# Optimization experiments

Measured on AMD Instinct MI355X. Metric: run time of the kernel, lower is better.

Reference implementation:

```python
import jax, jax.numpy as jnp
import numpy as np

N_POINTS = 200000
C_IN = 64
C_OUT = 64
K_VOL = 27  # 3x3x3 kernel offsets
N_PAIRS = 100000  # neighbor pairs per kernel offset
BN_EPS = 1e-5


def setup_inputs() -> dict:
    key = jax.random.key(0)
    k1, k2, k3, k4 = jax.random.split(key, 4)
    feats = jax.random.normal(k1, (N_POINTS, C_IN), dtype=jnp.float32)
    in_map = jax.random.randint(k2, (K_VOL, N_PAIRS), 0, N_POINTS, dtype=jnp.int32)
    out_map = jax.random.randint(k3, (K_VOL, N_PAIRS), 0, N_POINTS, dtype=jnp.int32)
    # learned params: conv kernel [K, Cin, Cout], BN affine + running stats
    kernel = jax.random.normal(k4, (K_VOL, C_IN, C_OUT), dtype=jnp.float32) * (1.0 / np.sqrt(C_IN * K_VOL))
    gamma = jnp.ones((C_OUT,), dtype=jnp.float32)
    beta = jnp.zeros((C_OUT,), dtype=jnp.float32)
    running_mean = jnp.zeros((C_OUT,), dtype=jnp.float32)
    running_var = jnp.ones((C_OUT,), dtype=jnp.float32)
    return {
        "feats": feats,
        "kernel": kernel,
        "gamma": gamma,
        "beta": beta,
        "running_mean": running_mean,
        "running_var": running_var,
        "in_map": in_map,
        "out_map": out_map,
    }


def reference(feats, kernel, gamma, beta, running_mean, running_var, in_map, out_map):
    # Sparse conv as gather -> per-offset GEMM -> scatter-add (torchsparse semantics)
    n = feats.shape[0]
    c_out = kernel.shape[-1]
    gathered = feats[in_map]                                   # [K, M, Cin]
    contrib = jnp.einsum('kmc,kco->kmo', gathered, kernel)     # [K, M, Cout]
    out = jnp.zeros((n, c_out), dtype=feats.dtype)
    out = out.at[out_map.reshape(-1)].add(contrib.reshape(-1, c_out))
    # BatchNorm (inference: fold running stats into scale/bias) + ReLU epilogue
    scale = gamma * jax.lax.rsqrt(running_var + BN_EPS)        # [Cout]
    out = out * scale + (beta - running_mean * scale)
    return jax.nn.relu(out)
```

## Files before the change

### kernel.cpp

```cpp
#include <hip/hip_runtime.h>
#include <hip/hip_bf16.h>

#define NPTS 200000
#define CIN 64
#define COUT 64
#define KVOL 27
#define NPAIRS 100000
#define GROUPS_PER_K (NPAIRS / 16)
#define GROUPS_PER_BLOCK 64
#define CHUNKS_PER_K ((GROUPS_PER_K + GROUPS_PER_BLOCK - 1) / GROUPS_PER_BLOCK)
#define BN_EPS 1e-5f

typedef __attribute__((ext_vector_type(8))) short short8;
typedef __attribute__((ext_vector_type(4))) float f32x4;

__device__ inline ushort f2bf(float x) {
    union { __hip_bfloat16 h; ushort u; } cv;
    cv.h = __float2bfloat16(x);
    return cv.u;
}

__global__ __launch_bounds__(256) void conv_scatter_kernel(
    const float* __restrict__ feats,
    const float* __restrict__ wk,
    const int* __restrict__ in_map,
    const int* __restrict__ out_map,
    float* __restrict__ accum)
{
    const int koff  = blockIdx.x / CHUNKS_PER_K;
    const int chunk = blockIdx.x % CHUNKS_PER_K;
    const int lane  = threadIdx.x & 63;
    const int wave  = threadIdx.x >> 6;
    const int m     = lane & 15;
    const int q     = lane >> 4;

    short8 bfrag[2][4];
    const float* wbase = wk + koff * (CIN * COUT);
    #pragma unroll
    for (int h = 0; h < 2; ++h) {
        #pragma unroll
        for (int nt = 0; nt < 4; ++nt) {
            #pragma unroll
            for (int e = 0; e < 8; ++e) {
                const int kin = h * 32 + q * 8 + e;
                bfrag[h][nt][e] = (short)f2bf(wbase[kin * COUT + nt * 16 + m]);
            }
        }
    }

    const int* imap = in_map + koff * NPAIRS;
    const int* omap = out_map + koff * NPAIRS;

    #pragma unroll 1
    for (int it = 0; it < GROUPS_PER_BLOCK / 4; ++it) {
        const int g = chunk * GROUPS_PER_BLOCK + it * 4 + wave;
        if (g >= GROUPS_PER_K) break;
        const int base = g * 16;

        const int row = imap[base + m];
        const float* fr = feats + (size_t)row * CIN + q * 8;
        const f32x4 f00 = *(const f32x4*)(fr);
        const f32x4 f01 = *(const f32x4*)(fr + 4);
        const f32x4 f10 = *(const f32x4*)(fr + 32);
        const f32x4 f11 = *(const f32x4*)(fr + 36);

        short8 a0, a1;
        #pragma unroll
        for (int e = 0; e < 4; ++e) {
            a0[e]     = (short)f2bf(f00[e]);
            a0[e + 4] = (short)f2bf(f01[e]);
            a1[e]     = (short)f2bf(f10[e]);
            a1[e + 4] = (short)f2bf(f11[e]);
        }

        f32x4 acc[4];
        #pragma unroll
        for (int nt = 0; nt < 4; ++nt) acc[nt] = (f32x4){0.f, 0.f, 0.f, 0.f};
        #pragma unroll
        for (int nt = 0; nt < 4; ++nt) {
            acc[nt] = __builtin_amdgcn_mfma_f32_16x16x32_bf16(a0, bfrag[0][nt], acc[nt], 0, 0, 0);
            acc[nt] = __builtin_amdgcn_mfma_f32_16x16x32_bf16(a1, bfrag[1][nt], acc[nt], 0, 0, 0);
        }

        int orow[4];
        #pragma unroll
        for (int r = 0; r < 4; ++r) orow[r] = omap[base + q * 4 + r];

        #pragma unroll
        for (int nt = 0; nt < 4; ++nt) {
            #pragma unroll
            for (int r = 0; r < 4; ++r) {
                unsafeAtomicAdd(accum + (size_t)orow[r] * COUT + nt * 16 + m, acc[nt][r]);
            }
        }
    }
}

__global__ __launch_bounds__(256) void bn_relu_kernel(
    const float* __restrict__ accum,
    const float* __restrict__ gamma,
    const float* __restrict__ beta,
    const float* __restrict__ rmean,
    const float* __restrict__ rvar,
    float* __restrict__ out)
{
    __shared__ float s_scale[COUT];
    __shared__ float s_bias[COUT];
    if (threadIdx.x < COUT) {
        const int c = threadIdx.x;
        const float sc = gamma[c] * rsqrtf(rvar[c] + BN_EPS);
        s_scale[c] = sc;
        s_bias[c]  = beta[c] - rmean[c] * sc;
    }
    __syncthreads();

    const int idx = (blockIdx.x * 256 + threadIdx.x) * 4;
    if (idx < NPTS * COUT) {
        const f32x4 v = *(const f32x4*)(accum + idx);
        const int c0 = idx & (COUT - 1);
        f32x4 o;
        #pragma unroll
        for (int e = 0; e < 4; ++e) {
            o[e] = fmaxf(v[e] * s_scale[c0 + e] + s_bias[c0 + e], 0.f);
        }
        *(f32x4*)(out + idx) = o;
    }
}

extern "C" void kernel_launch(void* const* d_in, const int* in_sizes, int n_in,
                              void* d_out, int out_size, void* d_ws, size_t ws_size,
                              hipStream_t stream) {
    const float* feats = (const float*)d_in[0];
    const float* wk    = (const float*)d_in[1];
    const float* gamma = (const float*)d_in[2];
    const float* beta  = (const float*)d_in[3];
    const float* rmean = (const float*)d_in[4];
    const float* rvar  = (const float*)d_in[5];
    const int* imap    = (const int*)d_in[6];
    const int* omap    = (const int*)d_in[7];
    float* out         = (float*)d_out;
    float* accum       = (float*)d_ws;

    hipMemsetAsync(accum, 0, (size_t)NPTS * COUT * sizeof(float), stream);

    conv_scatter_kernel<<<KVOL * CHUNKS_PER_K, 256, 0, stream>>>(feats, wk, imap, omap, accum);

    bn_relu_kernel<<<(NPTS * COUT / 4 + 255) / 256, 256, 0, stream>>>(
        accum, gamma, beta, rmean, rvar, out);
}
```

Baseline: 677.7 us.

## Replace global atomic scatter with output-tile bucketing and LDS gather-accumulate

Builds a counting-sort of neighbor pairs keyed by (16-row output tile, kernel offset) using a histogram, three-stage prefix scan and fill pass, then runs a gather-style conv where each wave owns one output tile and accumulates into LDS with shared-memory atomics. BN+ReLU is fused into the tile write-out, and weights are pre-transposed to bf16 once. This removes the 256MB-scale global float atomics, the memset and the separate BN pass. The cost is several extra small kernels, global integer atomics for bucketing, and partially filled MFMA groups, since buckets average about 8 pairs per 16-row slot.

Result: slower. 1.378 ms (+103.4%).

```diff
diff --git a/kernel.cpp b/kernel.cpp
--- a/kernel.cpp
+++ b/kernel.cpp
@@ -6,10 +6,16 @@
 #define COUT 64
 #define KVOL 27
 #define NPAIRS 100000
-#define GROUPS_PER_K (NPAIRS / 16)
-#define GROUPS_PER_BLOCK 64
-#define CHUNKS_PER_K ((GROUPS_PER_K + GROUPS_PER_BLOCK - 1) / GROUPS_PER_BLOCK)
+#define NPAIRS_TOT (KVOL * NPAIRS)
+#define NTILES (NPTS / 16)
+#define NKEYS (NTILES * KVOL)
+#define SCAN_ITEMS 2048
+#define NSCANB ((NKEYS + SCAN_ITEMS - 1) / SCAN_ITEMS)
 #define BN_EPS 1e-5f
+
+static_assert(NPTS % 16 == 0, "tiles");
+static_assert(NTILES % 4 == 0, "4 waves/block");
+static_assert(NSCANB <= 256, "single-block top scan");
 
 typedef __attribute__((ext_vector_type(8))) short short8;
 typedef __attribute__((ext_vector_type(4))) float f32x4;
@@ -20,110 +26,185 @@
     return cv.u;
 }
 
-__global__ __launch_bounds__(256) void conv_scatter_kernel(
+
+__global__ __launch_bounds__(256) void wprep_kernel(const float* __restrict__ wk,
+                                                    ushort* __restrict__ wt) {
+    const int i = blockIdx.x * 256 + threadIdx.x;
+    if (i >= KVOL * CIN * COUT) return;
+    const int k = i >> 12, r = i & 4095, co = r >> 6, ci = r & 63;
+    wt[i] = f2bf(wk[(k << 12) | (ci << 6) | co]);
+}
+
+__global__ __launch_bounds__(256) void hist_kernel(const int* __restrict__ omap,
+                                                   int* __restrict__ cnt) {
+    for (int i = blockIdx.x * 256 + threadIdx.x; i < NPAIRS_TOT; i += gridDim.x * 256) {
+        const int k = i / NPAIRS;
+        atomicAdd(&cnt[(omap[i] >> 4) * KVOL + k], 1);
+    }
+}
+
+__global__ __launch_bounds__(256) void scan1_kernel(const int* __restrict__ cnt,
+                                                    int* __restrict__ offs,
+                                                    int* __restrict__ bsum) {
+    __shared__ int s[256];
+    const int t = threadIdx.x;
+    const int base = blockIdx.x * SCAN_ITEMS + t * 8;
+    int v[8]; int sum = 0;
+    #pragma unroll
+    for (int i = 0; i < 8; ++i) {
+        const int idx = base + i;
+        v[i] = (idx < NKEYS) ? cnt[idx] : 0;
+        sum += v[i];
+    }
+    s[t] = sum;
+    __syncthreads();
+    for (int off = 1; off < 256; off <<= 1) {
+        const int x = (t >= off) ? s[t - off] : 0;
+        __syncthreads();
+        s[t] += x;
+        __syncthreads();
+    }
+    if (t == 255) bsum[blockIdx.x] = s[255];
+    int run = s[t] - sum;
+    #pragma unroll
+    for (int i = 0; i < 8; ++i) {
+        const int idx = base + i;
+        if (idx < NKEYS) offs[idx] = run;
+        run += v[i];
+    }
+}
+
+__global__ __launch_bounds__(256) void scan2_kernel(int* __restrict__ bsum) {
+    __shared__ int s[256];
+    const int t = threadIdx.x;
+    const int v = (t < NSCANB) ? bsum[t] : 0;
+    s[t] = v;
+    __syncthreads();
+    for (int off = 1; off < 256; off <<= 1) {
+        const int x = (t >= off) ? s[t - off] : 0;
+        __syncthreads();
+        s[t] += x;
+        __syncthreads();
+    }
+    if (t < NSCANB) bsum[t] = s[t] - v;
+}
+
+__global__ __launch_bounds__(256) void scan3_kernel(int* __restrict__ offs,
+                                                    int* __restrict__ cursor,
+                                                    const int* __restrict__ bsum) {
+    const int base = blockIdx.x * SCAN_ITEMS + threadIdx.x * 8;
+    const int add = bsum[blockIdx.x];
+    #pragma unroll
+    for (int i = 0; i < 8; ++i) {
+        const int idx = base + i;
+        if (idx < NKEYS) {
+            const int v = offs[idx] + add;
+            offs[idx] = v;
+            cursor[idx] = v;
+        }
+    }
+}
+
+__global__ __launch_bounds__(256) void fill_kernel(const int* __restrict__ imap,
+                                                   const int* __restrict__ omap,
+                                                   int* __restrict__ cursor,
+                                                   unsigned* __restrict__ payload) {
+    for (int i = blockIdx.x * 256 + threadIdx.x; i < NPAIRS_TOT; i += gridDim.x * 256) {
+        const int k = i / NPAIRS;
+        const int o = omap[i];
+        const int key = (o >> 4) * KVOL + k;
+        const int pos = atomicAdd(&cursor[key], 1);
+        payload[pos] = (unsigned)imap[i] | ((unsigned)(o & 15) << 18);
+    }
+}
+
+__global__ __launch_bounds__(256) void conv_gather_kernel(
     const float* __restrict__ feats,
-    const float* __restrict__ wk,
-    const int* __restrict__ in_map,
-    const int* __restrict__ out_map,
-    float* __restrict__ accum)
-{
-    const int koff  = blockIdx.x / CHUNKS_PER_K;
-    const int chunk = blockIdx.x % CHUNKS_PER_K;
-    const int lane  = threadIdx.x & 63;
-    const int wave  = threadIdx.x >> 6;
-    const int m     = lane & 15;
-    const int q     = lane >> 4;
-
-    short8 bfrag[2][4];
-    const float* wbase = wk + koff * (CIN * COUT);
-    #pragma unroll
-    for (int h = 0; h < 2; ++h) {
-        #pragma unroll
-        for (int nt = 0; nt < 4; ++nt) {
-            #pragma unroll
-            for (int e = 0; e < 8; ++e) {
-                const int kin = h * 32 + q * 8 + e;
-                bfrag[h][nt][e] = (short)f2bf(wbase[kin * COUT + nt * 16 + m]);
-            }
-        }
-    }
-
-    const int* imap = in_map + koff * NPAIRS;
-    const int* omap = out_map + koff * NPAIRS;
-
-    #pragma unroll 1
-    for (int it = 0; it < GROUPS_PER_BLOCK / 4; ++it) {
-        const int g = chunk * GROUPS_PER_BLOCK + it * 4 + wave;
-        if (g >= GROUPS_PER_K) break;
-        const int base = g * 16;
-
-        const int row = imap[base + m];
-        const float* fr = feats + (size_t)row * CIN + q * 8;
-        const f32x4 f00 = *(const f32x4*)(fr);
-        const f32x4 f01 = *(const f32x4*)(fr + 4);
-        const f32x4 f10 = *(const f32x4*)(fr + 32);
-        const f32x4 f11 = *(const f32x4*)(fr + 36);
-
-        short8 a0, a1;
-        #pragma unroll
-        for (int e = 0; e < 4; ++e) {
-            a0[e]     = (short)f2bf(f00[e]);
-            a0[e + 4] = (short)f2bf(f01[e]);
-            a1[e]     = (short)f2bf(f10[e]);
-            a1[e + 4] = (short)f2bf(f11[e]);
-        }
-
-        f32x4 acc[4];
-        #pragma unroll
-        for (int nt = 0; nt < 4; ++nt) acc[nt] = (f32x4){0.f, 0.f, 0.f, 0.f};
-        #pragma unroll
-        for (int nt = 0; nt < 4; ++nt) {
-            acc[nt] = __builtin_amdgcn_mfma_f32_16x16x32_bf16(a0, bfrag[0][nt], acc[nt], 0, 0, 0);
-            acc[nt] = __builtin_amdgcn_mfma_f32_16x16x32_bf16(a1, bfrag[1][nt], acc[nt], 0, 0, 0);
-        }
-
-        int orow[4];
-        #pragma unroll
-        for (int r = 0; r < 4; ++r) orow[r] = omap[base + q * 4 + r];
-
-        #pragma unroll
-        for (int nt = 0; nt < 4; ++nt) {
-            #pragma unroll
-            for (int r = 0; r < 4; ++r) {
-                unsafeAtomicAdd(accum + (size_t)orow[r] * COUT + nt * 16 + m, acc[nt][r]);
-            }
-        }
-    }
-}
-
-__global__ __launch_bounds__(256) void bn_relu_kernel(
-    const float* __restrict__ accum,
+    const ushort* __restrict__ wt,
+    const unsigned* __restrict__ payload,
+    const int* __restrict__ offs,
     const float* __restrict__ gamma,
     const float* __restrict__ beta,
     const float* __restrict__ rmean,
     const float* __restrict__ rvar,
     float* __restrict__ out)
 {
-    __shared__ float s_scale[COUT];
-    __shared__ float s_bias[COUT];
-    if (threadIdx.x < COUT) {
-        const int c = threadIdx.x;
-        const float sc = gamma[c] * rsqrtf(rvar[c] + BN_EPS);
-        s_scale[c] = sc;
-        s_bias[c]  = beta[c] - rmean[c] * sc;
-    }
+    __shared__ float tile[4][16 * 65];
+    const int lane = threadIdx.x & 63;
+    const int wave = threadIdx.x >> 6;
+    const int m = lane & 15;
+    const int q = lane >> 4;
+    const int t = blockIdx.x * 4 + wave;
+
+    for (int i = lane; i < 16 * 65; i += 64) tile[wave][i] = 0.f;
+
+    const float sc = gamma[lane] * rsqrtf(rvar[lane] + BN_EPS);
+    const float bi = beta[lane] - rmean[lane] * sc;
+
+    for (int k = 0; k < KVOL; ++k) {
+        short8 bfrag[2][4];
+        #pragma unroll
+        for (int h = 0; h < 2; ++h)
+            #pragma unroll
+            for (int nt = 0; nt < 4; ++nt)
+                bfrag[h][nt] = *(const short8*)(wt + ((k * 64 + nt * 16 + m) * 64 + h * 32 + q * 8));
+
+        const int key = t * KVOL + k;
+        const int e0 = offs[key];
+        const int e1 = (key + 1 < NKEYS) ? offs[key + 1] : NPAIRS_TOT;
+
+        for (int base = e0; base < e1; base += 16) {
+            const int ei = base + m;
+            const bool av = (ei < e1);
+            unsigned pl = 0u;
+            f32x4 f00 = (f32x4){0.f, 0.f, 0.f, 0.f}, f01 = f00, f10 = f00, f11 = f00;
+            if (av) {
+                pl = payload[ei];
+                const float* fr = feats + (size_t)(pl & 0x3FFFFu) * CIN + q * 8;
+                f00 = *(const f32x4*)(fr);
+                f01 = *(const f32x4*)(fr + 4);
+                f10 = *(const f32x4*)(fr + 32);
+                f11 = *(const f32x4*)(fr + 36);
+            }
+            short8 a0, a1;
+            #pragma unroll
+            for (int e = 0; e < 4; ++e) {
+                a0[e]     = (short)f2bf(f00[e]);
+                a0[e + 4] = (short)f2bf(f01[e]);
+                a1[e]     = (short)f2bf(f10[e]);
+                a1[e + 4] = (short)f2bf(f11[e]);
+            }
+
+            unsigned plr[4];
+            #pragma unroll
+            for (int r = 0; r < 4; ++r) plr[r] = (unsigned)__shfl((int)pl, q * 4 + r);
+
+            f32x4 acc[4];
+            #pragma unroll
+            for (int nt = 0; nt < 4; ++nt) acc[nt] = (f32x4){0.f, 0.f, 0.f, 0.f};
+            #pragma unroll
+            for (int nt = 0; nt < 4; ++nt) {
+                acc[nt] = __builtin_amdgcn_mfma_f32_16x16x32_bf16(a0, bfrag[0][nt], acc[nt], 0, 0, 0);
+                acc[nt] = __builtin_amdgcn_mfma_f32_16x16x32_bf16(a1, bfrag[1][nt], acc[nt], 0, 0, 0);
+            }
+
+            #pragma unroll
+            for (int r = 0; r < 4; ++r) {
+                if (base + q * 4 + r < e1) {
+                    const int l = (int)((plr[r] >> 18) & 15u);
+                    #pragma unroll
+                    for (int nt = 0; nt < 4; ++nt)
+                        atomicAdd(&tile[wave][l * 65 + nt * 16 + m], acc[nt][r]);
+                }
+            }
+        }
+    }
+
     __syncthreads();
-
-    const int idx = (blockIdx.x * 256 + threadIdx.x) * 4;
-    if (idx < NPTS * COUT) {
-        const f32x4 v = *(const f32x4*)(accum + idx);
-        const int c0 = idx & (COUT - 1);
-        f32x4 o;
-        #pragma unroll
-        for (int e = 0; e < 4; ++e) {
-            o[e] = fmaxf(v[e] * s_scale[c0 + e] + s_bias[c0 + e], 0.f);
-        }
-        *(f32x4*)(out + idx) = o;
+    #pragma unroll
+    for (int r = 0; r < 16; ++r) {
+        const float v = tile[wave][r * 65 + lane];
+        out[((size_t)t * 16 + r) * COUT + lane] = fmaxf(v * sc + bi, 0.f);
     }
 }
 
@@ -139,12 +220,22 @@
     const int* imap    = (const int*)d_in[6];
     const int* omap    = (const int*)d_in[7];
     float* out         = (float*)d_out;
-    float* accum       = (float*)d_ws;
-
-    hipMemsetAsync(accum, 0, (size_t)NPTS * COUT * sizeof(float), stream);
-
-    conv_scatter_kernel<<<KVOL * CHUNKS_PER_K, 256, 0, stream>>>(feats, wk, imap, omap, accum);
-
-    bn_relu_kernel<<<(NPTS * COUT / 4 + 255) / 256, 256, 0, stream>>>(
-        accum, gamma, beta, rmean, rvar, out);
-}
+
+    char* ws = (char*)d_ws;
+    int* cnt          = (int*)(ws);
+    int* offs         = (int*)(ws + (2u << 20));
+    int* bsum         = (int*)(ws + (4u << 20));
+    int* cursor       = (int*)(ws + (5u << 20));
+    ushort* wt        = (ushort*)(ws + (7u << 20));
+    unsigned* payload = (unsigned*)(ws + (8u << 20));
+
+    hipMemsetAsync(cnt, 0, NKEYS * sizeof(int), stream);
+    wprep_kernel<<<(KVOL * CIN * COUT + 255) / 256, 256, 0, stream>>>(wk, wt);
+    hist_kernel<<<2048, 256, 0, stream>>>(omap, cnt);
+    scan1_kernel<<<NSCANB, 256, 0, stream>>>(cnt, offs, bsum);
+    scan2_kernel<<<1, 256, 0, stream>>>(bsum);
+    scan3_kernel<<<NSCANB, 256, 0, stream>>>(offs, cursor, bsum);
+    fill_kernel<<<2048, 256, 0, stream>>>(imap, omap, cursor, payload);
+    conv_gather_kernel<<<NTILES / 4, 256, 0, stream>>>(
+        feats, wt, payload, offs, gamma, beta, rmean, rvar, out);
+}
```

## Use bf16 accumulator with packed bf16x2 atomics and pre-converted bf16 features

Applied to the files above, without the earlier changes.

Features are converted to bf16 once in a new prep kernel, so the conv kernel's gathers read half the bytes and skip per-use conversion. The scatter accumulator becomes bf16: lanes exchange values with a shuffle so each lane issues packed bf16x2 atomic adds, halving the atomic count and the accumulator traffic, memset and readback. The cost is accumulating up to dozens of contributions per point in bf16, which loses precision and may exceed tolerance.

After: 683.6 us. About the same (+0.9%).

```diff
diff --git a/kernel.cpp b/kernel.cpp
--- a/kernel.cpp
+++ b/kernel.cpp
@@ -11,6 +11,10 @@
 #define CHUNKS_PER_K ((GROUPS_PER_K + GROUPS_PER_BLOCK - 1) / GROUPS_PER_BLOCK)
 #define BN_EPS 1e-5f
 
+static_assert(NPAIRS % 16 == 0, "full chunks");
+static_assert(NPTS * CIN % (256 * 8) == 0, "fprep exact grid");
+static_assert((size_t)NPTS * COUT * 2 * 2 <= 51200000, "accum+fbuf fit in R0 ws");
+
 typedef __attribute__((ext_vector_type(8))) short short8;
 typedef __attribute__((ext_vector_type(4))) float f32x4;
 
@@ -20,12 +24,32 @@
     return cv.u;
 }
 
+__device__ inline void pk_atomic(ushort* p, float lo, float hi) {
+    union { uint u; __hip_bfloat162 h; } cv;
+    cv.u = (uint)f2bf(lo) | ((uint)f2bf(hi) << 16);
+    unsafeAtomicAdd((__hip_bfloat162*)p, cv.h);
+}
+
+__global__ __launch_bounds__(256) void fprep_kernel(const float* __restrict__ feats,
+                                                    ushort* __restrict__ fbuf) {
+    const int i = blockIdx.x * 256 + threadIdx.x;
+    const f32x4 v0 = *(const f32x4*)(feats + (size_t)i * 8);
+    const f32x4 v1 = *(const f32x4*)(feats + (size_t)i * 8 + 4);
+    short8 o;
+    #pragma unroll
+    for (int e = 0; e < 4; ++e) {
+        o[e]     = (short)f2bf(v0[e]);
+        o[e + 4] = (short)f2bf(v1[e]);
+    }
+    *(short8*)(fbuf + (size_t)i * 8) = o;
+}
+
 __global__ __launch_bounds__(256) void conv_scatter_kernel(
-    const float* __restrict__ feats,
+    const ushort* __restrict__ fbuf,
     const float* __restrict__ wk,
-    const int* __restrict__ in_map,
-    const int* __restrict__ out_map,
-    float* __restrict__ accum)
+    const int* __restrict__ imap,
+    const int* __restrict__ omap,
+    ushort* __restrict__ accum)
 {
     const int koff  = blockIdx.x / CHUNKS_PER_K;
     const int chunk = blockIdx.x % CHUNKS_PER_K;
@@ -37,19 +61,16 @@
     short8 bfrag[2][4];
     const float* wbase = wk + koff * (CIN * COUT);
     #pragma unroll
-    for (int h = 0; h < 2; ++h) {
+    for (int h = 0; h < 2; ++h)
         #pragma unroll
-        for (int nt = 0; nt < 4; ++nt) {
+        for (int nt = 0; nt < 4; ++nt)
             #pragma unroll
-            for (int e = 0; e < 8; ++e) {
-                const int kin = h * 32 + q * 8 + e;
-                bfrag[h][nt][e] = (short)f2bf(wbase[kin * COUT + nt * 16 + m]);
-            }
-        }
-    }
+            for (int e = 0; e < 8; ++e)
+                bfrag[h][nt][e] = (short)f2bf(wbase[(h * 32 + q * 8 + e) * COUT + nt * 16 + m]);
 
-    const int* imap = in_map + koff * NPAIRS;
-    const int* omap = out_map + koff * NPAIRS;
+    const int* im = imap + koff * NPAIRS;
+    const int* om = omap + koff * NPAIRS;
+    const bool ev = (m & 1) == 0;
 
     #pragma unroll 1
     for (int it = 0; it < GROUPS_PER_BLOCK / 4; ++it) {
@@ -57,21 +78,14 @@
         if (g >= GROUPS_PER_K) break;
         const int base = g * 16;
 
-        const int row = imap[base + m];
-        const float* fr = feats + (size_t)row * CIN + q * 8;
-        const f32x4 f00 = *(const f32x4*)(fr);
-        const f32x4 f01 = *(const f32x4*)(fr + 4);
-        const f32x4 f10 = *(const f32x4*)(fr + 32);
-        const f32x4 f11 = *(const f32x4*)(fr + 36);
+        const int row = im[base + m];
+        const ushort* fr = fbuf + (size_t)row * CIN + q * 8;
+        const short8 a0 = *(const short8*)(fr);
+        const short8 a1 = *(const short8*)(fr + 32);
 
-        short8 a0, a1;
+        int orow[4];
         #pragma unroll
-        for (int e = 0; e < 4; ++e) {
-            a0[e]     = (short)f2bf(f00[e]);
-            a0[e + 4] = (short)f2bf(f01[e]);
-            a1[e]     = (short)f2bf(f10[e]);
-            a1[e + 4] = (short)f2bf(f11[e]);
-        }
+        for (int r = 0; r < 4; ++r) orow[r] = om[base + q * 4 + r];
 
         f32x4 acc[4];
         #pragma unroll
@@ -82,22 +96,25 @@
             acc[nt] = __builtin_amdgcn_mfma_f32_16x16x32_bf16(a1, bfrag[1][nt], acc[nt], 0, 0, 0);
         }
 
-        int orow[4];
-        #pragma unroll
-        for (int r = 0; r < 4; ++r) orow[r] = omap[base + q * 4 + r];
-
+        const size_t r0 = (size_t)(ev ? orow[0] : orow[2]) * COUT;
+        const size_t r1 = (size_t)(ev ? orow[1] : orow[3]) * COUT;
         #pragma unroll
         for (int nt = 0; nt < 4; ++nt) {
-            #pragma unroll
-            for (int r = 0; r < 4; ++r) {
-                unsafeAtomicAdd(accum + (size_t)orow[r] * COUT + nt * 16 + m, acc[nt][r]);
-            }
+            const float c0 = __shfl_xor(acc[nt][0], 1);
+            const float c1 = __shfl_xor(acc[nt][1], 1);
+            const float c2 = __shfl_xor(acc[nt][2], 1);
+            const float c3 = __shfl_xor(acc[nt][3], 1);
+            const float s0lo = ev ? acc[nt][0] : c2,  s0hi = ev ? c0 : acc[nt][2];
+            const float s1lo = ev ? acc[nt][1] : c3,  s1hi = ev ? c1 : acc[nt][3];
+            const int cb = nt * 16 + (m & 14);
+            pk_atomic(accum + r0 + cb, s0lo, s0hi);
+            pk_atomic(accum + r1 + cb, s1lo, s1hi);
         }
     }
 }
 
 __global__ __launch_bounds__(256) void bn_relu_kernel(
-    const float* __restrict__ accum,
+    const ushort* __restrict__ accum,
     const float* __restrict__ gamma,
     const float* __restrict__ beta,
     const float* __restrict__ rmean,
@@ -114,17 +131,20 @@
     }
     __syncthreads();
 
-    const int idx = (blockIdx.x * 256 + threadIdx.x) * 4;
-    if (idx < NPTS * COUT) {
-        const f32x4 v = *(const f32x4*)(accum + idx);
-        const int c0 = idx & (COUT - 1);
-        f32x4 o;
-        #pragma unroll
-        for (int e = 0; e < 4; ++e) {
-            o[e] = fmaxf(v[e] * s_scale[c0 + e] + s_bias[c0 + e], 0.f);
-        }
-        *(f32x4*)(out + idx) = o;
+    const size_t idx = ((size_t)blockIdx.x * 256 + threadIdx.x) * 8;
+    const short8 v = *(const short8*)(accum + idx);
+    const int c0 = (int)(idx & (COUT - 1));
+    f32x4 o0, o1;
+    #pragma unroll
+    for (int e = 0; e < 4; ++e) {
+        union { uint u; float f; } lo, hi;
+        lo.u = ((uint)(ushort)v[e]) << 16;
+        hi.u = ((uint)(ushort)v[e + 4]) << 16;
+        o0[e] = fmaxf(lo.f * s_scale[c0 + e]     + s_bias[c0 + e],     0.f);
+        o1[e] = fmaxf(hi.f * s_scale[c0 + e + 4] + s_bias[c0 + e + 4], 0.f);
     }
+    *(f32x4*)(out + idx)     = o0;
+    *(f32x4*)(out + idx + 4) = o1;
 }
 
 extern "C" void kernel_launch(void* const* d_in, const int* in_sizes, int n_in,
@@ -139,12 +159,13 @@
     const int* imap    = (const int*)d_in[6];
     const int* omap    = (const int*)d_in[7];
     float* out         = (float*)d_out;
-    float* accum       = (float*)d_ws;
 
-    hipMemsetAsync(accum, 0, (size_t)NPTS * COUT * sizeof(float), stream);
+    ushort* accum = (ushort*)d_ws;
+    ushort* fbuf  = (ushort*)((char*)d_ws + (size_t)NPTS * COUT * 2);
 
-    conv_scatter_kernel<<<KVOL * CHUNKS_PER_K, 256, 0, stream>>>(feats, wk, imap, omap, accum);
-
-    bn_relu_kernel<<<(NPTS * COUT / 4 + 255) / 256, 256, 0, stream>>>(
+    hipMemsetAsync(accum, 0, (size_t)NPTS * COUT * sizeof(ushort), stream);
+    fprep_kernel<<<NPTS * CIN / (256 * 8), 256, 0, stream>>>(feats, fbuf);
+    conv_scatter_kernel<<<KVOL * CHUNKS_PER_K, 256, 0, stream>>>(fbuf, wk, imap, omap, accum);
+    bn_relu_kernel<<<NPTS * COUT / (256 * 8), 256, 0, stream>>>(
         accum, gamma, beta, rmean, rvar, out);
 }
```
